# Kernel tuning notes

Measured on AMD Instinct MI355X. Metric: run time of the kernel, lower is better.

## Reference

```python
import jax, jax.numpy as jnp
import numpy as np

N_SRC, N_TGT, N_EDGES = 100000, 50000, 600000
IN_CH, OUT_CH = 128, 128
NUM_EDGE_TYPES, NUM_NODE_TYPES = 7, 4


def setup_inputs() -> dict:
    key = jax.random.key(0)
    ks = jax.random.split(key, 9)
    x_src = jax.random.normal(ks[0], (N_SRC, IN_CH), dtype=jnp.float32)
    x_target = jax.random.normal(ks[1], (N_TGT, IN_CH), dtype=jnp.float32)
    # PyG Linear: y = x @ W.T (+ b); W has shape (out, in)
    rel_w = jax.random.normal(ks[2], (NUM_EDGE_TYPES, OUT_CH, IN_CH), dtype=jnp.float32) * 0.05
    root_w = jax.random.normal(ks[3], (NUM_NODE_TYPES, OUT_CH, IN_CH), dtype=jnp.float32) * 0.05
    root_b = jax.random.normal(ks[4], (NUM_NODE_TYPES, OUT_CH), dtype=jnp.float32) * 0.05
    edge_src = jax.random.randint(ks[5], (N_EDGES,), 0, N_SRC, dtype=jnp.int32)
    edge_dst = jax.random.randint(ks[6], (N_EDGES,), 0, N_TGT, dtype=jnp.int32)
    edge_type = jax.random.randint(ks[7], (N_EDGES,), 0, NUM_EDGE_TYPES, dtype=jnp.int32)
    target_node_type = jax.random.randint(ks[8], (N_TGT,), 0, NUM_NODE_TYPES, dtype=jnp.int32)
    return {
        "x_src": x_src, "x_target": x_target,
        "rel_w": rel_w, "root_w": root_w, "root_b": root_b,
        "edge_src": edge_src, "edge_dst": edge_dst,
        "edge_type": edge_type, "target_node_type": target_node_type,
    }


def reference(x_src, x_target, rel_w, root_w, root_b,
              edge_src, edge_dst, edge_type, target_node_type):
    n_tgt = x_target.shape[0]
    num_rel = rel_w.shape[0]
    num_ntypes = root_w.shape[0]
    # Gather source features once for all edges: (E, in)
    msg = x_src[edge_src]
    out = jnp.zeros((n_tgt, rel_w.shape[1]), dtype=x_target.dtype)
    # Per-relation linear transform + scatter-MEAN over that relation's edges
    # (matches one propagate(aggr='mean') call per edge type: nodes with no
    #  incoming edges of type r contribute 0 for that relation).
    for r in range(num_rel):
        mask = (edge_type == r).astype(msg.dtype)  # (E,)
        y = (msg * mask[:, None]) @ rel_w[r].T     # (E, out)
        s = jax.ops.segment_sum(y, edge_dst, num_segments=n_tgt)
        cnt = jax.ops.segment_sum(mask, edge_dst, num_segments=n_tgt)
        out = out + s / jnp.maximum(cnt, 1.0)[:, None]
    # Per-node-type root linear (with bias), masked add
    for t in range(num_ntypes):
        m = (target_node_type == t)
        root = x_target @ root_w[t].T + root_b[t]
        out = out + jnp.where(m[:, None], root, 0.0)
    return out
```

## Files before the change

### kernel.cpp

```cpp
#include <hip/hip_runtime.h>

#define NSRC 100000
#define NTGT 50000
#define NE   600000
#define CH   128
#define NREL 7
#define NTYP 4
#define NP   (NREL * NTGT)
#define NB   ((NP + 1023) / 1024)
#define NBLK ((NTGT + 63) / 64)

typedef __attribute__((ext_vector_type(4))) float f32x4;
typedef __attribute__((ext_vector_type(8))) short bf16x8;
typedef unsigned int uint;
typedef unsigned short ushort;

static constexpr long long NXB4 = (long long)NSRC * CH / 4;
static constexpr long long NXT4 = (long long)NTGT * CH / 4;
static constexpr long long NWR4 = (long long)NREL * CH * CH / 4;
static constexpr long long NWT4 = (long long)NTYP * CH * CH / 4;
static constexpr int CONVB  = (int)((NXB4 + NXT4 + NWR4 + NWT4 + 255) / 256);
static constexpr int COUNTB = (NE + 255) / 256;

static constexpr size_t A256(size_t x) { return (x + 255) & ~(size_t)255; }
static constexpr size_t CNT_O   = 0;
static constexpr size_t EOFF_O  = A256(CNT_O + (size_t)NP * 4);
static constexpr size_t CUR_O   = A256(EOFF_O + (size_t)NP * 4);
static constexpr size_t SEDGE_O = A256(CUR_O + (size_t)NP * 4);
static constexpr size_t SDST_O  = A256(SEDGE_O + (size_t)NE * 4);
static constexpr size_t WB_O    = A256(SDST_O + (size_t)NE * 4);
static constexpr size_t XB_O    = A256(WB_O + (size_t)(NREL + NTYP) * CH * CH * 2);
static constexpr size_t XTB_O   = A256(XB_O + (size_t)NSRC * CH * 2);

__device__ __forceinline__ uint bfpack(float a, float b) {
  uint ua = __float_as_uint(a); ua = (ua + 0x7fff + ((ua >> 16) & 1)) >> 16;
  uint ub = __float_as_uint(b); ub = (ub + 0x7fff + ((ub >> 16) & 1)) >> 16;
  return ua | (ub << 16);
}
__device__ __forceinline__ ushort f2b(float x) {
  uint u = __float_as_uint(x);
  return (ushort)((u + 0x7fff + ((u >> 16) & 1)) >> 16);
}
__device__ __forceinline__ float bl(uint u) { return __uint_as_float(u << 16); }
__device__ __forceinline__ float bh(uint u) { return __uint_as_float(u & 0xffff0000u); }

__global__ __launch_bounds__(256) void k_pre1(
    const float* __restrict__ xsrc, const float* __restrict__ xt,
    const float* __restrict__ relw, const float* __restrict__ rootw,
    ushort* __restrict__ xb, ushort* __restrict__ xtb, ushort* __restrict__ wb,
    const int* __restrict__ edst, const int* __restrict__ etyp, int* __restrict__ cnt) {
  int bx = blockIdx.x;
  if (bx < CONVB) {
    long long i4 = (long long)bx * 256 + threadIdx.x;
    const float* src; ushort* dst; long long off;
    if (i4 < NXB4) { src = xsrc; dst = xb; off = i4; }
    else if (i4 < NXB4 + NXT4) { src = xt; dst = xtb; off = i4 - NXB4; }
    else if (i4 < NXB4 + NXT4 + NWR4) { src = relw; dst = wb; off = i4 - NXB4 - NXT4; }
    else if (i4 < NXB4 + NXT4 + NWR4 + NWT4) {
      src = rootw; dst = wb + (size_t)NREL * CH * CH; off = i4 - NXB4 - NXT4 - NWR4;
    } else return;
    float4 v = *(const float4*)(src + off * 4);
    uint lo = (uint)f2b(v.x) | ((uint)f2b(v.y) << 16);
    uint hi = (uint)f2b(v.z) | ((uint)f2b(v.w) << 16);
    uint2 o = make_uint2(lo, hi);
    *(uint2*)(dst + off * 4) = o;
    return;
  }
  bx -= CONVB;
  int i = bx * 256 + threadIdx.x;
  if (i < NE) atomicAdd(&cnt[etyp[i] * NTGT + edst[i]], 1);
}

__global__ __launch_bounds__(256) void k_s1(const int* __restrict__ cnt,
                                            int* __restrict__ bsE) {
  __shared__ int sE[256];
  int t = threadIdx.x, p0 = blockIdx.x * 1024 + t * 4;
  int e = 0;
#pragma unroll
  for (int j = 0; j < 4; ++j) {
    int p = p0 + j;
    if (p < NP) e += cnt[p];
  }
  sE[t] = e; __syncthreads();
  for (int s = 128; s > 0; s >>= 1) {
    if (t < s) sE[t] += sE[t + s];
    __syncthreads();
  }
  if (t == 0) bsE[blockIdx.x] = sE[0];
}

__global__ __launch_bounds__(512) void k_s2(const int* __restrict__ bsE,
                                            int* __restrict__ bbE) {
  __shared__ int sE[512];
  int t = threadIdx.x;
  int e = (t < NB) ? bsE[t] : 0;
  sE[t] = e; __syncthreads();
  for (int s = 1; s < 512; s <<= 1) {
    int ae = 0;
    if (t >= s) ae = sE[t - s];
    __syncthreads();
    sE[t] += ae;
    __syncthreads();
  }
  if (t < NB) bbE[t] = sE[t] - e;
}

__global__ __launch_bounds__(256) void k_s3(const int* __restrict__ cnt,
    const int* __restrict__ bbE, int* __restrict__ eoff, int* __restrict__ cur) {
  __shared__ int sE[256];
  int t = threadIdx.x, p0 = blockIdx.x * 1024 + t * 4;
  int c[4]; int e = 0;
#pragma unroll
  for (int j = 0; j < 4; ++j) {
    int p = p0 + j;
    c[j] = (p < NP) ? cnt[p] : 0;
    e += c[j];
  }
  sE[t] = e; __syncthreads();
  for (int s = 1; s < 256; s <<= 1) {
    int ae = 0;
    if (t >= s) ae = sE[t - s];
    __syncthreads();
    sE[t] += ae;
    __syncthreads();
  }
  int baseE = bbE[blockIdx.x] + sE[t] - e;
#pragma unroll
  for (int j = 0; j < 4; ++j) {
    int p = p0 + j;
    if (p < NP) {
      eoff[p] = baseE;
      cur[p] = baseE;
      baseE += c[j];
    }
  }
}

__global__ __launch_bounds__(256) void k_esort(
    const int* __restrict__ esrc, const int* __restrict__ edst,
    const int* __restrict__ etyp, int* __restrict__ cur,
    int* __restrict__ sedge, int* __restrict__ sdst) {
  int i = blockIdx.x * 256 + threadIdx.x;
  if (i < NE) {
    int p = etyp[i] * NTGT + edst[i];
    int pos = atomicAdd(&cur[p], 1);
    sedge[pos] = esrc[i];
    sdst[pos] = edst[i];
  }
}

__device__ __forceinline__ void mfma_acc(const ushort* strip, const ushort* W,
                                         int m, int quad, f32x4* acc) {
  bf16x8 aF[4];
#pragma unroll
  for (int ks = 0; ks < 4; ++ks) {
    int c = ks * 4 + quad;
    aF[ks] = *(const bf16x8*)&strip[(m * 16 + (c ^ m)) << 3];
  }
#pragma unroll
  for (int ct = 0; ct < 8; ++ct) {
    int n = ct * 16 + m;
#pragma unroll
    for (int ks = 0; ks < 4; ++ks) {
      bf16x8 bF = *(const bf16x8*)(W + (size_t)n * CH + ks * 32 + quad * 8);
      acc[ct] = __builtin_amdgcn_mfma_f32_16x16x32_bf16(aF[ks], bF, acc[ct], 0, 0, 0);
    }
  }
}

__global__ __launch_bounds__(256) void k_mega(const ushort* __restrict__ xb,
    const ushort* __restrict__ xtb, const ushort* __restrict__ wb,
    const int* __restrict__ cnt, const int* __restrict__ eoff,
    const int* __restrict__ sedge, const int* __restrict__ sdst,
    const int* __restrict__ ntyp, const float* __restrict__ rootb,
    float* __restrict__ out) {
  __shared__ float accs[4 * 16 * CH];
  int wv = threadIdx.x >> 6, ln = threadIdx.x & 63;
  float* accw = accs + wv * (16 * CH);
  ushort* strip = (ushort*)accw;
  int m = ln & 15, quad = ln >> 4;

  int dstbase = blockIdx.x * 64 + wv * 16;
  if (dstbase >= NTGT) return;
  int nvalid = NTGT - dstbase; if (nvalid > 16) nvalid = 16;

  f32x4 acc[8];
#pragma unroll
  for (int ct = 0; ct < 8; ++ct) acc[ct] = (f32x4){0.f, 0.f, 0.f, 0.f};

  for (int rel = 0; rel < NREL; ++rel) {
    int p0 = rel * NTGT + dstbase;
    int pend = p0 + nvalid;
    int e0 = __builtin_amdgcn_readfirstlane(eoff[p0]);
    int e1 = __builtin_amdgcn_readfirstlane((pend < NP) ? eoff[pend] : NE);
    if (e1 <= e0) continue;

#pragma unroll
    for (int it = 0; it < 8; ++it)
      *(f32x4*)&accw[it * 256 + (ln << 2)] = (f32x4){0.f, 0.f, 0.f, 0.f};

    int e = e0;
    for (; e + 8 <= e1; e += 8) {
      int s[8], rr[8];
#pragma unroll
      for (int k = 0; k < 8; ++k) {
        s[k] = __builtin_amdgcn_readfirstlane(sedge[e + k]);
        rr[k] = __builtin_amdgcn_readfirstlane(sdst[e + k]) - dstbase;
      }
      uint u[8];
#pragma unroll
      for (int k = 0; k < 8; ++k)
        u[k] = *(const uint*)(xb + (size_t)s[k] * CH + (ln << 1));
#pragma unroll
      for (int k = 0; k < 8; ++k) {
        float* a = &accw[rr[k] * CH + (ln << 1)];
        float2 v = *(float2*)a;
        v.x += bl(u[k]); v.y += bh(u[k]);
        *(float2*)a = v;
      }
    }
    for (; e < e1; ++e) {
      int s = __builtin_amdgcn_readfirstlane(sedge[e]);
      int rr = __builtin_amdgcn_readfirstlane(sdst[e]) - dstbase;
      uint u = *(const uint*)(xb + (size_t)s * CH + (ln << 1));
      float* a = &accw[rr * CH + (ln << 1)];
      float2 v = *(float2*)a;
      v.x += bl(u); v.y += bh(u);
      *(float2*)a = v;
    }

    uint wpk[16];
#pragma unroll
    for (int i = 0; i < 16; ++i) {
      int n = (i < nvalid) ? cnt[p0 + i] : 0;
      float inv = (n > 0) ? __builtin_amdgcn_rcpf((float)n) : 0.f;
      float2 a = *(const float2*)&accw[i * CH + (ln << 1)];
      wpk[i] = bfpack(a.x * inv, a.y * inv);
    }
#pragma unroll
    for (int i = 0; i < 16; ++i) {
      int c = ln >> 2;
      *(uint*)&strip[((i * 16 + (c ^ i)) << 3) + ((ln & 3) << 1)] = wpk[i];
    }
    mfma_acc(strip, wb + (size_t)rel * CH * CH, m, quad, acc);
  }

  for (int t = 0; t < NTYP; ++t) {
#pragma unroll
    for (int i = 0; i < 16; ++i) {
      int dst = dstbase + i;
      uint w = 0;
      if (i < nvalid && ntyp[dst] == t)
        w = *(const uint*)(xtb + (size_t)dst * CH + (ln << 1));
      int c = ln >> 2;
      *(uint*)&strip[((i * 16 + (c ^ i)) << 3) + ((ln & 3) << 1)] = w;
    }
    mfma_acc(strip, wb + (size_t)(NREL + t) * CH * CH, m, quad, acc);
  }

#pragma unroll
  for (int reg = 0; reg < 4; ++reg) {
    int dst = dstbase + quad * 4 + reg;
    if (dst < NTGT) {
      int t = ntyp[dst];
#pragma unroll
      for (int ct = 0; ct < 8; ++ct) {
        int col = ct * 16 + m;
        out[(size_t)dst * CH + col] = acc[ct][reg] + rootb[(size_t)t * CH + col];
      }
    }
  }
}

extern "C" void kernel_launch(void* const* d_in, const int* in_sizes, int n_in,
                              void* d_out, int out_size, void* d_ws, size_t ws_size,
                              hipStream_t stream) {
  (void)in_sizes; (void)n_in; (void)out_size; (void)ws_size;
  const float* xsrc  = (const float*)d_in[0];
  const float* xt    = (const float*)d_in[1];
  const float* relw  = (const float*)d_in[2];
  const float* rootw = (const float*)d_in[3];
  const float* rootb = (const float*)d_in[4];
  const int* esrc = (const int*)d_in[5];
  const int* edst = (const int*)d_in[6];
  const int* etyp = (const int*)d_in[7];
  const int* ntyp = (const int*)d_in[8];
  float* out = (float*)d_out;

  char* ws = (char*)d_ws;
  int*   cnt    = (int*)(ws + CNT_O);
  int*   eoff   = (int*)(ws + EOFF_O);
  int*   cur    = (int*)(ws + CUR_O);
  int*   sedge  = (int*)(ws + SEDGE_O);
  int*   sdst   = (int*)(ws + SDST_O);
  ushort* wb    = (ushort*)(ws + WB_O);
  ushort* xb    = (ushort*)(ws + XB_O);
  ushort* xtb   = (ushort*)(ws + XTB_O);

  hipMemsetAsync(cnt, 0, (size_t)NP * 4, stream);
  k_pre1<<<dim3(CONVB + COUNTB), dim3(256), 0, stream>>>(
      xsrc, xt, relw, rootw, xb, xtb, wb, edst, etyp, cnt);
  k_s1<<<dim3(NB), dim3(256), 0, stream>>>(cnt, (int*)(ws + EOFF_O));
  k_s2<<<dim3(1), dim3(512), 0, stream>>>((int*)(ws + EOFF_O), (int*)(ws + CUR_O));
  k_s3<<<dim3(NB), dim3(256), 0, stream>>>(cnt, (int*)(ws + CUR_O), eoff, cur);
  k_esort<<<dim3(COUNTB), dim3(256), 0, stream>>>(esrc, edst, etyp, cur, sedge, sdst);
  k_mega<<<dim3(NBLK), dim3(256), 0, stream>>>(
      xb, xtb, wb, cnt, eoff, sedge, sdst, ntyp, rootb, out);
}
```

Baseline: 414.9 us.

## Rework aggregation to per-row register accumulation and fuse scan/sort/convert kernels

The main kernel now handles 8 destination rows per wave instead of 16. Each 16-lane group accumulates one destination's neighbour features in registers using 16-byte bf16 loads, with a one-step prefetch of the next source row, replacing the shared-memory float accumulator and per-edge readfirstlane loop. The scan's second and third stages are merged into one kernel, and the edge sort is fused with the bf16 conversion. The sorted-destination array and the count array are dropped, with counts taken from eoff differences. The cost is half the MFMA tile going unused (8 of 16 rows) and load imbalance when the in-degrees within a wave differ.

```diff
diff --git a/kernel.cpp b/kernel.cpp
--- a/kernel.cpp
+++ b/kernel.cpp
@@ -8,7 +8,7 @@
 #define NTYP 4
 #define NP   (NREL * NTGT)
 #define NB   ((NP + 1023) / 1024)
-#define NBLK ((NTGT + 63) / 64)
+#define NBLK ((NTGT + 31) / 32)
 
 typedef __attribute__((ext_vector_type(4))) float f32x4;
 typedef __attribute__((ext_vector_type(8))) short bf16x8;
@@ -24,11 +24,11 @@
 
 static constexpr size_t A256(size_t x) { return (x + 255) & ~(size_t)255; }
 static constexpr size_t CNT_O   = 0;
-static constexpr size_t EOFF_O  = A256(CNT_O + (size_t)NP * 4);
-static constexpr size_t CUR_O   = A256(EOFF_O + (size_t)NP * 4);
+static constexpr size_t BSE_O   = A256(CNT_O + (size_t)NP * 4);
+static constexpr size_t EOFF_O  = A256(BSE_O + (size_t)NB * 4);
+static constexpr size_t CUR_O   = A256(EOFF_O + (size_t)(NP + 1) * 4);
 static constexpr size_t SEDGE_O = A256(CUR_O + (size_t)NP * 4);
-static constexpr size_t SDST_O  = A256(SEDGE_O + (size_t)NE * 4);
-static constexpr size_t WB_O    = A256(SDST_O + (size_t)NE * 4);
+static constexpr size_t WB_O    = A256(SEDGE_O + (size_t)NE * 4);
 static constexpr size_t XB_O    = A256(WB_O + (size_t)(NREL + NTYP) * CH * CH * 2);
 static constexpr size_t XTB_O   = A256(XB_O + (size_t)NSRC * CH * 2);
 
@@ -44,30 +44,17 @@
 __device__ __forceinline__ float bl(uint u) { return __uint_as_float(u << 16); }
 __device__ __forceinline__ float bh(uint u) { return __uint_as_float(u & 0xffff0000u); }
 
-__global__ __launch_bounds__(256) void k_pre1(
-    const float* __restrict__ xsrc, const float* __restrict__ xt,
-    const float* __restrict__ relw, const float* __restrict__ rootw,
-    ushort* __restrict__ xb, ushort* __restrict__ xtb, ushort* __restrict__ wb,
-    const int* __restrict__ edst, const int* __restrict__ etyp, int* __restrict__ cnt) {
-  int bx = blockIdx.x;
-  if (bx < CONVB) {
-    long long i4 = (long long)bx * 256 + threadIdx.x;
-    const float* src; ushort* dst; long long off;
-    if (i4 < NXB4) { src = xsrc; dst = xb; off = i4; }
-    else if (i4 < NXB4 + NXT4) { src = xt; dst = xtb; off = i4 - NXB4; }
-    else if (i4 < NXB4 + NXT4 + NWR4) { src = relw; dst = wb; off = i4 - NXB4 - NXT4; }
-    else if (i4 < NXB4 + NXT4 + NWR4 + NWT4) {
-      src = rootw; dst = wb + (size_t)NREL * CH * CH; off = i4 - NXB4 - NXT4 - NWR4;
-    } else return;
-    float4 v = *(const float4*)(src + off * 4);
-    uint lo = (uint)f2b(v.x) | ((uint)f2b(v.y) << 16);
-    uint hi = (uint)f2b(v.z) | ((uint)f2b(v.w) << 16);
-    uint2 o = make_uint2(lo, hi);
-    *(uint2*)(dst + off * 4) = o;
-    return;
-  }
-  bx -= CONVB;
-  int i = bx * 256 + threadIdx.x;
+__device__ __forceinline__ void add8(float* a, uint4 u) {
+  a[0] += bl(u.x); a[1] += bh(u.x);
+  a[2] += bl(u.y); a[3] += bh(u.y);
+  a[4] += bl(u.z); a[5] += bh(u.z);
+  a[6] += bl(u.w); a[7] += bh(u.w);
+}
+
+__global__ __launch_bounds__(256) void k_count(const int* __restrict__ edst,
+                                               const int* __restrict__ etyp,
+                                               int* __restrict__ cnt) {
+  int i = blockIdx.x * 256 + threadIdx.x;
   if (i < NE) atomicAdd(&cnt[etyp[i] * NTGT + edst[i]], 1);
 }
 
@@ -89,64 +76,71 @@
   if (t == 0) bsE[blockIdx.x] = sE[0];
 }
 
-__global__ __launch_bounds__(512) void k_s2(const int* __restrict__ bsE,
-                                            int* __restrict__ bbE) {
+__global__ __launch_bounds__(512) void k_s23(const int* __restrict__ cnt,
+                                             const int* __restrict__ bsE,
+                                             int* __restrict__ eoff,
+                                             int* __restrict__ cur) {
   __shared__ int sE[512];
+  __shared__ int sBase;
   int t = threadIdx.x;
   int e = (t < NB) ? bsE[t] : 0;
   sE[t] = e; __syncthreads();
   for (int s = 1; s < 512; s <<= 1) {
-    int ae = 0;
-    if (t >= s) ae = sE[t - s];
-    __syncthreads();
-    sE[t] += ae;
-    __syncthreads();
-  }
-  if (t < NB) bbE[t] = sE[t] - e;
-}
-
-__global__ __launch_bounds__(256) void k_s3(const int* __restrict__ cnt,
-    const int* __restrict__ bbE, int* __restrict__ eoff, int* __restrict__ cur) {
-  __shared__ int sE[256];
-  int t = threadIdx.x, p0 = blockIdx.x * 1024 + t * 4;
-  int c[4]; int e = 0;
-#pragma unroll
-  for (int j = 0; j < 4; ++j) {
-    int p = p0 + j;
-    c[j] = (p < NP) ? cnt[p] : 0;
-    e += c[j];
-  }
-  sE[t] = e; __syncthreads();
-  for (int s = 1; s < 256; s <<= 1) {
-    int ae = 0;
-    if (t >= s) ae = sE[t - s];
-    __syncthreads();
-    sE[t] += ae;
-    __syncthreads();
-  }
-  int baseE = bbE[blockIdx.x] + sE[t] - e;
-#pragma unroll
-  for (int j = 0; j < 4; ++j) {
-    int p = p0 + j;
-    if (p < NP) {
-      eoff[p] = baseE;
-      cur[p] = baseE;
-      baseE += c[j];
+    int a = 0; if (t >= s) a = sE[t - s];
+    __syncthreads();
+    sE[t] += a;
+    __syncthreads();
+  }
+  if (t == blockIdx.x) sBase = sE[t] - e;
+  __syncthreads();
+  int base0 = sBase;
+  int p0 = blockIdx.x * 1024 + t * 2;
+  int c0 = (p0 < NP) ? cnt[p0] : 0;
+  int c1 = (p0 + 1 < NP) ? cnt[p0 + 1] : 0;
+  int e2 = c0 + c1;
+  sE[t] = e2; __syncthreads();
+  for (int s = 1; s < 512; s <<= 1) {
+    int a = 0; if (t >= s) a = sE[t - s];
+    __syncthreads();
+    sE[t] += a;
+    __syncthreads();
+  }
+  int baseE = base0 + sE[t] - e2;
+  if (p0 < NP)     { eoff[p0] = baseE;     cur[p0] = baseE; }
+  if (p0 + 1 < NP) { eoff[p0 + 1] = baseE + c0; cur[p0 + 1] = baseE + c0; }
+  if (p0 + 1 == NP - 1) eoff[NP] = baseE + c0 + c1;
+}
+
+__global__ __launch_bounds__(256) void k_esconv(
+    const int* __restrict__ esrc, const int* __restrict__ edst,
+    const int* __restrict__ etyp, int* __restrict__ cur, int* __restrict__ sedge,
+    const float* __restrict__ xsrc, const float* __restrict__ xt,
+    const float* __restrict__ relw, const float* __restrict__ rootw,
+    ushort* __restrict__ xb, ushort* __restrict__ xtb, ushort* __restrict__ wb) {
+  int bx = blockIdx.x;
+  if (bx < COUNTB) {
+    int i = bx * 256 + threadIdx.x;
+    if (i < NE) {
+      int p = etyp[i] * NTGT + edst[i];
+      int pos = atomicAdd(&cur[p], 1);
+      sedge[pos] = esrc[i];
     }
-  }
-}
-
-__global__ __launch_bounds__(256) void k_esort(
-    const int* __restrict__ esrc, const int* __restrict__ edst,
-    const int* __restrict__ etyp, int* __restrict__ cur,
-    int* __restrict__ sedge, int* __restrict__ sdst) {
-  int i = blockIdx.x * 256 + threadIdx.x;
-  if (i < NE) {
-    int p = etyp[i] * NTGT + edst[i];
-    int pos = atomicAdd(&cur[p], 1);
-    sedge[pos] = esrc[i];
-    sdst[pos] = edst[i];
-  }
+    return;
+  }
+  bx -= COUNTB;
+  long long i4 = (long long)bx * 256 + threadIdx.x;
+  const float* src; ushort* dst; long long off;
+  if (i4 < NXB4) { src = xsrc; dst = xb; off = i4; }
+  else if (i4 < NXB4 + NXT4) { src = xt; dst = xtb; off = i4 - NXB4; }
+  else if (i4 < NXB4 + NXT4 + NWR4) { src = relw; dst = wb; off = i4 - NXB4 - NXT4; }
+  else if (i4 < NXB4 + NXT4 + NWR4 + NWT4) {
+    src = rootw; dst = wb + (size_t)NREL * CH * CH; off = i4 - NXB4 - NXT4 - NWR4;
+  } else return;
+  float4 v = *(const float4*)(src + off * 4);
+  uint lo = (uint)f2b(v.x) | ((uint)f2b(v.y) << 16);
+  uint hi = (uint)f2b(v.z) | ((uint)f2b(v.w) << 16);
+  uint2 o = make_uint2(lo, hi);
+  *(uint2*)(dst + off * 4) = o;
 }
 
 __device__ __forceinline__ void mfma_acc(const ushort* strip, const ushort* W,
@@ -168,21 +162,20 @@
   }
 }
 
-__global__ __launch_bounds__(256) void k_mega(const ushort* __restrict__ xb,
+__global__ __launch_bounds__(256, 4) void k_mega(const ushort* __restrict__ xb,
     const ushort* __restrict__ xtb, const ushort* __restrict__ wb,
-    const int* __restrict__ cnt, const int* __restrict__ eoff,
-    const int* __restrict__ sedge, const int* __restrict__ sdst,
+    const int* __restrict__ eoff, const int* __restrict__ sedge,
     const int* __restrict__ ntyp, const float* __restrict__ rootb,
     float* __restrict__ out) {
-  __shared__ float accs[4 * 16 * CH];
+  __shared__ ushort As[4 * 16 * CH];
   int wv = threadIdx.x >> 6, ln = threadIdx.x & 63;
-  float* accw = accs + wv * (16 * CH);
-  ushort* strip = (ushort*)accw;
+  ushort* strip = As + wv * (16 * CH);
+  int q = ln >> 4;
+  int t = ln & 15;
   int m = ln & 15, quad = ln >> 4;
 
-  int dstbase = blockIdx.x * 64 + wv * 16;
+  int dstbase = blockIdx.x * 32 + wv * 8;
   if (dstbase >= NTGT) return;
-  int nvalid = NTGT - dstbase; if (nvalid > 16) nvalid = 16;
 
   f32x4 acc[8];
 #pragma unroll
@@ -190,83 +183,97 @@
 
   for (int rel = 0; rel < NREL; ++rel) {
     int p0 = rel * NTGT + dstbase;
-    int pend = p0 + nvalid;
-    int e0 = __builtin_amdgcn_readfirstlane(eoff[p0]);
-    int e1 = __builtin_amdgcn_readfirstlane((pend < NP) ? eoff[pend] : NE);
-    if (e1 <= e0) continue;
-
-#pragma unroll
-    for (int it = 0; it < 8; ++it)
-      *(f32x4*)&accw[it * 256 + (ln << 2)] = (f32x4){0.f, 0.f, 0.f, 0.f};
-
-    int e = e0;
-    for (; e + 8 <= e1; e += 8) {
-      int s[8], rr[8];
-#pragma unroll
-      for (int k = 0; k < 8; ++k) {
-        s[k] = __builtin_amdgcn_readfirstlane(sedge[e + k]);
-        rr[k] = __builtin_amdgcn_readfirstlane(sdst[e + k]) - dstbase;
+    int ev = 0;
+    if (ln < 9) ev = eoff[p0 + ln];
+    int eA0 = __shfl(ev, q),     eA1 = __shfl(ev, q + 1);
+    int eB0 = __shfl(ev, q + 4), eB1 = __shfl(ev, q + 5);
+    int etot = __shfl(ev, 8) - __shfl(ev, 0);
+    if (etot == 0) continue;
+    int na = eA1 - eA0, nb = eB1 - eB0;
+
+    float accA[8], accB[8];
+#pragma unroll
+    for (int c = 0; c < 8; ++c) { accA[c] = 0.f; accB[c] = 0.f; }
+
+    int u = max(na, nb);
+    u = max(u, __shfl_xor(u, 16));
+    u = max(u, __shfl_xor(u, 32));
+
+    for (int base = 0; base < u; base += 16) {
+      int ca = min(na - base, 16); if (ca < 0) ca = 0;
+      int cb = min(nb - base, 16); if (cb < 0) cb = 0;
+      int sidxA = (t < ca) ? sedge[eA0 + base + t] : 0;
+      int sidxB = (t < cb) ? sedge[eB0 + base + t] : 0;
+      int cmax = u - base; if (cmax > 16) cmax = 16;
+
+      uint4 va = {0, 0, 0, 0}, vb = {0, 0, 0, 0};
+      bool la = (0 < ca), lb = (0 < cb);
+      if (la) {
+        int s = __shfl(sidxA, (q << 4));
+        va = *(const uint4*)(xb + (size_t)s * CH + (t << 3));
       }
-      uint u[8];
-#pragma unroll
-      for (int k = 0; k < 8; ++k)
-        u[k] = *(const uint*)(xb + (size_t)s[k] * CH + (ln << 1));
-#pragma unroll
-      for (int k = 0; k < 8; ++k) {
-        float* a = &accw[rr[k] * CH + (ln << 1)];
-        float2 v = *(float2*)a;
-        v.x += bl(u[k]); v.y += bh(u[k]);
-        *(float2*)a = v;
+      if (lb) {
+        int s = __shfl(sidxB, (q << 4));
+        vb = *(const uint4*)(xb + (size_t)s * CH + (t << 3));
+      }
+      for (int j = 0; j < cmax; ++j) {
+        uint4 ua = va, ub = vb;
+        bool pa = la, pb = lb;
+        la = (j + 1 < ca); lb = (j + 1 < cb);
+        if (la) {
+          int s = __shfl(sidxA, (q << 4) + j + 1);
+          va = *(const uint4*)(xb + (size_t)s * CH + (t << 3));
+        }
+        if (lb) {
+          int s = __shfl(sidxB, (q << 4) + j + 1);
+          vb = *(const uint4*)(xb + (size_t)s * CH + (t << 3));
+        }
+        if (pa) add8(accA, ua);
+        if (pb) add8(accB, ub);
       }
     }
-    for (; e < e1; ++e) {
-      int s = __builtin_amdgcn_readfirstlane(sedge[e]);
-      int rr = __builtin_amdgcn_readfirstlane(sdst[e]) - dstbase;
-      uint u = *(const uint*)(xb + (size_t)s * CH + (ln << 1));
-      float* a = &accw[rr * CH + (ln << 1)];
-      float2 v = *(float2*)a;
-      v.x += bl(u); v.y += bh(u);
-      *(float2*)a = v;
-    }
-
-    uint wpk[16];
-#pragma unroll
-    for (int i = 0; i < 16; ++i) {
-      int n = (i < nvalid) ? cnt[p0 + i] : 0;
-      float inv = (n > 0) ? __builtin_amdgcn_rcpf((float)n) : 0.f;
-      float2 a = *(const float2*)&accw[i * CH + (ln << 1)];
-      wpk[i] = bfpack(a.x * inv, a.y * inv);
-    }
-#pragma unroll
-    for (int i = 0; i < 16; ++i) {
-      int c = ln >> 2;
-      *(uint*)&strip[((i * 16 + (c ^ i)) << 3) + ((ln & 3) << 1)] = wpk[i];
-    }
+
+    float invA = (na > 0) ? __builtin_amdgcn_rcpf((float)na) : 0.f;
+    float invB = (nb > 0) ? __builtin_amdgcn_rcpf((float)nb) : 0.f;
+    uint4 wA, wB;
+    wA.x = bfpack(accA[0] * invA, accA[1] * invA);
+    wA.y = bfpack(accA[2] * invA, accA[3] * invA);
+    wA.z = bfpack(accA[4] * invA, accA[5] * invA);
+    wA.w = bfpack(accA[6] * invA, accA[7] * invA);
+    wB.x = bfpack(accB[0] * invB, accB[1] * invB);
+    wB.y = bfpack(accB[2] * invB, accB[3] * invB);
+    wB.z = bfpack(accB[4] * invB, accB[5] * invB);
+    wB.w = bfpack(accB[6] * invB, accB[7] * invB);
+    *(uint4*)&strip[(q * 16 + (t ^ q)) << 3] = wA;
+    *(uint4*)&strip[((q + 4) * 16 + (t ^ (q + 4))) << 3] = wB;
+
     mfma_acc(strip, wb + (size_t)rel * CH * CH, m, quad, acc);
   }
 
-  for (int t = 0; t < NTYP; ++t) {
-#pragma unroll
-    for (int i = 0; i < 16; ++i) {
-      int dst = dstbase + i;
-      uint w = 0;
-      if (i < nvalid && ntyp[dst] == t)
-        w = *(const uint*)(xtb + (size_t)dst * CH + (ln << 1));
-      int c = ln >> 2;
-      *(uint*)&strip[((i * 16 + (c ^ i)) << 3) + ((ln & 3) << 1)] = w;
-    }
-    mfma_acc(strip, wb + (size_t)(NREL + t) * CH * CH, m, quad, acc);
+  int dA = dstbase + q, dB = dstbase + q + 4;
+  uint4 xrA = *(const uint4*)(xtb + (size_t)dA * CH + (t << 3));
+  uint4 xrB = *(const uint4*)(xtb + (size_t)dB * CH + (t << 3));
+  int ntA = ntyp[dA], ntB = ntyp[dB];
+  const uint4 z4 = {0, 0, 0, 0};
+  for (int ty = 0; ty < NTYP; ++ty) {
+    uint4 wA = (ntA == ty) ? xrA : z4;
+    uint4 wB = (ntB == ty) ? xrB : z4;
+    *(uint4*)&strip[(q * 16 + (t ^ q)) << 3] = wA;
+    *(uint4*)&strip[((q + 4) * 16 + (t ^ (q + 4))) << 3] = wB;
+    mfma_acc(strip, wb + (size_t)(NREL + ty) * CH * CH, m, quad, acc);
   }
 
 #pragma unroll
   for (int reg = 0; reg < 4; ++reg) {
-    int dst = dstbase + quad * 4 + reg;
-    if (dst < NTGT) {
-      int t = ntyp[dst];
+    int row = quad * 4 + reg;
+    if (row < 8) {
+      int dst = dstbase + row;
+      int tt = ntyp[dst];
+      const float* rb = rootb + (size_t)tt * CH;
 #pragma unroll
       for (int ct = 0; ct < 8; ++ct) {
         int col = ct * 16 + m;
-        out[(size_t)dst * CH + col] = acc[ct][reg] + rootb[(size_t)t * CH + col];
+        out[(size_t)dst * CH + col] = acc[ct][reg] + rb[col];
       }
     }
   }
@@ -289,21 +296,20 @@
 
   char* ws = (char*)d_ws;
   int*   cnt    = (int*)(ws + CNT_O);
+  int*   bsE    = (int*)(ws + BSE_O);
   int*   eoff   = (int*)(ws + EOFF_O);
   int*   cur    = (int*)(ws + CUR_O);
   int*   sedge  = (int*)(ws + SEDGE_O);
-  int*   sdst   = (int*)(ws + SDST_O);
   ushort* wb    = (ushort*)(ws + WB_O);
   ushort* xb    = (ushort*)(ws + XB_O);
   ushort* xtb   = (ushort*)(ws + XTB_O);
 
   hipMemsetAsync(cnt, 0, (size_t)NP * 4, stream);
-  k_pre1<<<dim3(CONVB + COUNTB), dim3(256), 0, stream>>>(
-      xsrc, xt, relw, rootw, xb, xtb, wb, edst, etyp, cnt);
-  k_s1<<<dim3(NB), dim3(256), 0, stream>>>(cnt, (int*)(ws + EOFF_O));
-  k_s2<<<dim3(1), dim3(512), 0, stream>>>((int*)(ws + EOFF_O), (int*)(ws + CUR_O));
-  k_s3<<<dim3(NB), dim3(256), 0, stream>>>(cnt, (int*)(ws + CUR_O), eoff, cur);
-  k_esort<<<dim3(COUNTB), dim3(256), 0, stream>>>(esrc, edst, etyp, cur, sedge, sdst);
+  k_count<<<dim3(COUNTB), dim3(256), 0, stream>>>(edst, etyp, cnt);
+  k_s1<<<dim3(NB), dim3(256), 0, stream>>>(cnt, bsE);
+  k_s23<<<dim3(NB), dim3(512), 0, stream>>>(cnt, bsE, eoff, cur);
+  k_esconv<<<dim3(COUNTB + CONVB), dim3(256), 0, stream>>>(
+      esrc, edst, etyp, cur, sedge, xsrc, xt, relw, rootw, xb, xtb, wb);
   k_mega<<<dim3(NBLK), dim3(256), 0, stream>>>(
-      xb, xtb, wb, cnt, eoff, sedge, sdst, ntyp, rootb, out);
-}
+      xb, xtb, wb, eoff, sedge, ntyp, rootb, out);
+}
```

Result: slower. 518.4 us (+24.9%).
